# Kernel tuning notes

Hardware: AMD Instinct MI355X
Metric: run time of the kernel (lower is better)

The kernel has to match this reference:

```python
import jax, jax.numpy as jnp
import numpy as np

FP4_AMAX = 6.0
FP8_AMAX = 448.0
E2M1_LUT = jnp.array([0.0, 0.5, 1.0, 1.5, 2.0, 3.0, 4.0, 6.0], dtype=jnp.float32)
# (threshold, code) pairs; applied in order, alternating <= and < comparisons
THRESHOLDS = [(5.0, 6), (3.5, 5), (2.5, 4), (1.75, 3), (1.25, 2), (0.75, 1), (0.25, 0)]


def _fp4_code(a):
    # a: abs-values, float32. Round-to-e2m1 magnitude code per the torch threshold table.
    code = jnp.full(a.shape, 7, dtype=jnp.int32)
    for i, (m, c) in enumerate(THRESHOLDS):
        mask = (a <= m) if i % 2 == 0 else (a < m)
        code = jnp.where(mask, c, code)
    return code


def simulate_nvfp4_quantize(w):
    # w: (out, in), in % 16 == 0. Returns fake-quantized weight, same shape/dtype.
    out_f, in_f = w.shape
    wb = w.reshape(out_f, in_f // 16, 16).astype(jnp.float32)
    gs = (FP4_AMAX * FP8_AMAX) / jnp.max(jnp.abs(wb))          # global fp32 scale
    s_decb = jnp.max(jnp.abs(wb), axis=-1) / FP4_AMAX           # per-16-block decode scale
    xs = jnp.clip(s_decb * gs, -FP8_AMAX, FP8_AMAX).astype(jnp.float8_e4m3fn)  # fp8 block scales
    xs_f = xs.astype(jnp.float32)
    s_encb = gs / jnp.clip(xs_f, 1e-12, None)                   # encode scale per block
    x_scaled = wb * s_encb[..., None]
    sign = jnp.where(jnp.signbit(x_scaled), -1.0, 1.0)
    mag = E2M1_LUT[_fp4_code(jnp.abs(x_scaled))]
    wq = sign * mag * (xs_f / gs)[..., None]                    # dequantize
    return wq.reshape(out_f, in_f).astype(w.dtype)


def setup_inputs() -> dict:
    key = jax.random.key(0)
    k1, k2, k3 = jax.random.split(key, 3)
    B, S, IN, OUT = 4, 2048, 4096, 4096
    x = jax.random.normal(k1, (B, S, IN), dtype=jnp.float32)
    weight = jax.random.normal(k2, (OUT, IN), dtype=jnp.float32) * 0.02
    bias = jax.random.normal(k3, (OUT,), dtype=jnp.float32) * 0.01
    return {"x": x, "weight": weight, "bias": bias}


def reference(x, weight, bias):
    # STE quantization: forward uses fake-quant weight
    weight_q = simulate_nvfp4_quantize(weight)
    # F.linear: x @ W^T + b
    return jnp.einsum("bsi,oi->bso", x, weight_q) + bias
```

## Files before the change

### kernel.cpp

```cpp
#include <hip/hip_runtime.h>
#include <hip/hip_bf16.h>
#include <stdint.h>

typedef __bf16 bf16_t;
typedef __bf16 bf16x8 __attribute__((ext_vector_type(8)));
typedef float  f32x4  __attribute__((ext_vector_type(4)));

#define BM 256
#define BN 256
#define BK 64
#define NTHREADS 512

__global__ void k_absmax(const float* __restrict__ w, unsigned int* __restrict__ out_bits, int n4) {
    int i = blockIdx.x * blockDim.x + threadIdx.x;
    int stride = gridDim.x * blockDim.x;
    const float4* w4 = (const float4*)w;
    float m = 0.0f;
    for (; i < n4; i += stride) {
        float4 v = w4[i];
        m = fmaxf(m, fmaxf(fmaxf(fabsf(v.x), fabsf(v.y)), fmaxf(fabsf(v.z), fabsf(v.w))));
    }
    #pragma unroll
    for (int off = 32; off; off >>= 1)
        m = fmaxf(m, __shfl_xor(m, off));
    if ((threadIdx.x & 63) == 0)
        atomicMax(out_bits, __float_as_uint(m));
}

__device__ __forceinline__ float e4m3_rne(float v) {
    if (v < 0.015625f) {
        return rintf(v * 512.0f) * (1.0f / 512.0f);
    }
    unsigned int u = __float_as_uint(v);
    unsigned int keep = u >> 20;
    unsigned int r = u & 0xFFFFFu;
    if (r > 0x80000u || (r == 0x80000u && (keep & 1u))) keep++;
    return __uint_as_float(keep << 20);
}

__global__ void k_quantize(const float* __restrict__ w, bf16_t* __restrict__ wq,
                           const unsigned int* __restrict__ maxbits, int nblk) {
    int t = blockIdx.x * blockDim.x + threadIdx.x;
    if (t >= nblk) return;
    float gmax = __uint_as_float(*maxbits);
    float gs = 2688.0f / gmax;
    const float4* w4 = (const float4*)w + (size_t)t * 4;
    float4 v0 = w4[0], v1 = w4[1], v2 = w4[2], v3 = w4[3];
    float vv[16];
    vv[0]=v0.x; vv[1]=v0.y; vv[2]=v0.z; vv[3]=v0.w;
    vv[4]=v1.x; vv[5]=v1.y; vv[6]=v1.z; vv[7]=v1.w;
    vv[8]=v2.x; vv[9]=v2.y; vv[10]=v2.z; vv[11]=v2.w;
    vv[12]=v3.x; vv[13]=v3.y; vv[14]=v3.z; vv[15]=v3.w;
    float bmax = 0.0f;
    #pragma unroll
    for (int j = 0; j < 16; ++j) bmax = fmaxf(bmax, fabsf(vv[j]));
    float s_decb = bmax / 6.0f;
    float xs_in  = fminf(s_decb * gs, 448.0f);
    float xs_f   = e4m3_rne(xs_in);
    float s_encb = gs / fmaxf(xs_f, 1e-12f);
    float dscale = xs_f / gs;
    bf16x8 o0, o1;
    #pragma unroll
    for (int j = 0; j < 16; ++j) {
        float xsc = vv[j] * s_encb;
        float a = fabsf(xsc);
        float mag = (a <= 0.25f) ? 0.0f
                  : (a <  0.75f) ? 0.5f
                  : (a <= 1.25f) ? 1.0f
                  : (a <  1.75f) ? 1.5f
                  : (a <= 2.5f ) ? 2.0f
                  : (a <  3.5f ) ? 3.0f
                  : (a <= 5.0f ) ? 4.0f : 6.0f;
        float sgn = __builtin_copysignf(1.0f, xsc);
        float val = (sgn * mag) * dscale;
        if (j < 8) o0[j] = (bf16_t)val; else o1[j - 8] = (bf16_t)val;
    }
    *(bf16x8*)(wq + (size_t)t * 16)     = o0;
    *(bf16x8*)(wq + (size_t)t * 16 + 8) = o1;
}

__global__ void k_cvt_x(const float* __restrict__ x, bf16_t* __restrict__ xb, long n8) {
    long i = blockIdx.x * (long)blockDim.x + threadIdx.x;
    long stride = (long)gridDim.x * blockDim.x;
    const float4* x4 = (const float4*)x;
    for (; i < n8; i += stride) {
        float4 a = x4[2 * i], b = x4[2 * i + 1];
        bf16x8 o;
        o[0] = (bf16_t)a.x; o[1] = (bf16_t)a.y; o[2] = (bf16_t)a.z; o[3] = (bf16_t)a.w;
        o[4] = (bf16_t)b.x; o[5] = (bf16_t)b.y; o[6] = (bf16_t)b.z; o[7] = (bf16_t)b.w;
        *(bf16x8*)(xb + i * 8) = o;
    }
}

__device__ __forceinline__ void BARRIER() {
    asm volatile("" ::: "memory");
    __builtin_amdgcn_s_barrier();
    asm volatile("" ::: "memory");
}

__device__ __forceinline__ void gload16(const bf16_t* g, bf16_t* l) {
    __builtin_amdgcn_global_load_lds(
        (const __attribute__((address_space(1))) unsigned int*)g,
        (__attribute__((address_space(3))) unsigned int*)l,
        16, 0, 0);
}

__global__ __launch_bounds__(NTHREADS, 2) void k_gemm(
        const bf16_t* __restrict__ A,
        const bf16_t* __restrict__ Bt,
        const float*  __restrict__ bias,
        float* __restrict__ C, int M, int N, int K) {
    __shared__ __align__(16) bf16_t sA[2][BM * BK];
    __shared__ __align__(16) bf16_t sB[2][BN * BK];

    int bid = blockIdx.x;
    int cpx = gridDim.x >> 3;
    int swz = (bid & 7) * cpx + (bid >> 3);
    int nbn = N / BN;
    int m0 = (swz / nbn) * BM, n0 = (swz % nbn) * BN;

    int tid  = threadIdx.x;
    int lane = tid & 63;
    int w    = tid >> 6;
    int wr   = w >> 2, wc = w & 3;
    int fr15 = lane & 15;
    int kg   = lane >> 4;

    int rowin = tid >> 3;
    int pg    = tid & 7;
    int gsw   = pg ^ (rowin & 7);
    int gstg[2], lstg[2];
    #pragma unroll
    for (int l = 0; l < 2; ++l) {
        gstg[l] = (l * 128 + rowin) * K + gsw * 8;
        lstg[l] = (l * 128 + rowin) * 64 + pg * 8;
    }
    int tq0 = tid >> 8;
    int rB  = (tid >> 3) & 31;
    int gbstg[2], lbstg[2];
    #pragma unroll
    for (int l = 0; l < 2; ++l) {
        int q = l * 2 + tq0;
        gbstg[l] = (q * 64 + rB) * K + gsw * 8;
        lbstg[l] = (q * 64 + rB) * 64 + pg * 8;
    }
    const bf16_t* Ab = A  + (size_t)m0 * K;
    const bf16_t* Bb = Bt + (size_t)n0 * K;

#define STGA(BUF, H, KT) do {                                                      \
        gload16(Ab + (H) * 64 * K + gstg[0] + (KT), &sA[BUF][(H) * 4096 + lstg[0]]); \
        gload16(Ab + (H) * 64 * K + gstg[1] + (KT), &sA[BUF][(H) * 4096 + lstg[1]]); \
    } while (0)
#define STGB(BUF, H, KT) do {                                                      \
        gload16(Bb + (H) * 32 * K + gbstg[0] + (KT), &sB[BUF][(H) * 2048 + lbstg[0]]); \
        gload16(Bb + (H) * 32 * K + gbstg[1] + (KT), &sB[BUF][(H) * 2048 + lbstg[1]]); \
    } while (0)

    int f01 = fr15 & 3, f2 = (fr15 >> 2) & 1;
    int pgr0 = 4 * (0 ^ f2) + (kg ^ f01);
    int pgr1 = 4 * (1 ^ f2) + (kg ^ f01);
    int baseA0 = (wr * 128 + fr15) * 64 + pgr0 * 8;
    int baseA1 = (wr * 128 + fr15) * 64 + pgr1 * 8;
    int baseB0 = (wc * 64  + fr15) * 64 + pgr0 * 8;
    int baseB1 = (wc * 64  + fr15) * 64 + pgr1 * 8;

    f32x4 acc[8][4] = {};
    bf16x8 afr[4][2];
    bf16x8 bfr[4][2];

    const int NT = K / BK;
    const int ITERS = NT / 2;

    STGB(0, 0, 0);  STGB(0, 1, 0);
    STGA(0, 0, 0);  STGA(0, 1, 0);
    STGB(1, 0, BK); STGB(1, 1, BK);
    STGA(1, 0, BK);
    asm volatile("s_waitcnt vmcnt(6)" ::: "memory");
    BARRIER();

#define RDA4(PA, MH) do {                                                          \
        _Pragma("unroll")                                                          \
        for (int m = 0; m < 4; ++m)                                                \
            afr[m][0] = *(const bf16x8*)((PA) + baseA0 + ((MH) * 4 + m) * 1024);   \
        _Pragma("unroll")                                                          \
        for (int m = 0; m < 4; ++m)                                                \
            afr[m][1] = *(const bf16x8*)((PA) + baseA1 + ((MH) * 4 + m) * 1024);   \
    } while (0)

#define RDB2(PB, NH) do {                                                          \
        _Pragma("unroll")                                                          \
        for (int j = 0; j < 2; ++j)                                                \
            bfr[(NH)*2+j][0] = *(const bf16x8*)((PB) + baseB0 + ((NH)*2+j) * 1024);\
        _Pragma("unroll")                                                          \
        for (int j = 0; j < 2; ++j)                                                \
            bfr[(NH)*2+j][1] = *(const bf16x8*)((PB) + baseB1 + ((NH)*2+j) * 1024);\
    } while (0)

#define MFQ(MH, NH) do {                                                                            \
        __builtin_amdgcn_s_setprio(1);                                                              \
        _Pragma("unroll")                                                                           \
        for (int n = 0; n < 2; ++n)                                                                 \
            _Pragma("unroll")                                                                       \
            for (int m = 0; m < 4; ++m)                                                             \
                acc[(MH)*4+m][(NH)*2+n] = __builtin_amdgcn_mfma_f32_16x16x32_bf16(                  \
                    afr[m][0], bfr[(NH)*2+n][0], acc[(MH)*4+m][(NH)*2+n], 0, 0, 0);                 \
        _Pragma("unroll")                                                                           \
        for (int n = 0; n < 2; ++n)                                                                 \
            _Pragma("unroll")                                                                       \
            for (int m = 0; m < 4; ++m)                                                             \
                acc[(MH)*4+m][(NH)*2+n] = __builtin_amdgcn_mfma_f32_16x16x32_bf16(                  \
                    afr[m][1], bfr[(NH)*2+n][1], acc[(MH)*4+m][(NH)*2+n], 0, 0, 0);                 \
        __builtin_amdgcn_s_setprio(0);                                                              \
    } while (0)

    RDA4(sA[0], 0); RDB2(sB[0], 0);

    for (int it = 0; it < ITERS; ++it) {
        const bool nl = (it + 1 < ITERS);
        const int ktB1 = (2 * it + 1) * BK;
        const int kt2  = (2 * it + 2) * BK;
        const int kt3  = (2 * it + 3) * BK;

        MFQ(0, 0);
        RDB2(sB[0], 1);
        STGA(1, 1, ktB1);
        BARRIER();

        MFQ(0, 1);
        RDA4(sA[0], 1);
        if (nl) STGB(0, 0, kt2);
        BARRIER();

        MFQ(1, 0);
        if (nl) STGB(0, 1, kt2);
        if (nl) { asm volatile("s_waitcnt vmcnt(6)" ::: "memory"); }
        else    { asm volatile("s_waitcnt vmcnt(2)" ::: "memory"); }
        BARRIER();

        MFQ(1, 1);
        if (nl) STGA(0, 0, kt2);
        if (nl) { asm volatile("s_waitcnt vmcnt(6)" ::: "memory"); }
        else    { asm volatile("s_waitcnt vmcnt(0)" ::: "memory"); }
        RDA4(sA[1], 0); RDB2(sB[1], 0);
        BARRIER();

        MFQ(0, 0);
        RDB2(sB[1], 1);
        if (nl) STGA(0, 1, kt2);
        BARRIER();

        MFQ(0, 1);
        RDA4(sA[1], 1);
        if (nl) STGB(1, 0, kt3);
        BARRIER();

        MFQ(1, 0);
        if (nl) STGB(1, 1, kt3);
        asm volatile("s_waitcnt vmcnt(6)" ::: "memory");
        BARRIER();

        MFQ(1, 1);
        if (nl) {
            STGA(1, 0, kt3);
            asm volatile("s_waitcnt vmcnt(6)" ::: "memory");
            RDA4(sA[0], 0); RDB2(sB[0], 0);
        }
        BARRIER();
    }
    asm volatile("s_waitcnt vmcnt(0)" ::: "memory");

    int crow = (lane >> 4) * 4;
    int ccol = lane & 15;
    float bv[4];
    #pragma unroll
    for (int j = 0; j < 4; ++j) bv[j] = bias[n0 + wc * 64 + j * 16 + ccol];
    #pragma unroll
    for (int i = 0; i < 8; ++i) {
        size_t mrow = (size_t)(m0 + wr * 128 + i * 16 + crow);
        #pragma unroll
        for (int j = 0; j < 4; ++j) {
            float* cp = C + mrow * N + (n0 + wc * 64 + j * 16 + ccol);
            #pragma unroll
            for (int r = 0; r < 4; ++r)
                cp[(size_t)r * N] = acc[i][j][r] + bv[j];
        }
    }
#undef STGA
#undef STGB
#undef RDA4
#undef RDB2
#undef MFQ
}

extern "C" void kernel_launch(void* const* d_in, const int* in_sizes, int n_in,
                              void* d_out, int out_size, void* d_ws, size_t ws_size,
                              hipStream_t stream) {
    const float* x    = (const float*)d_in[0];
    const float* wgt  = (const float*)d_in[1];
    const float* bias = (const float*)d_in[2];
    float* out = (float*)d_out;

    const int N = in_sizes[2];
    const int K = in_sizes[1] / N;
    const int M = in_sizes[0] / K;

    unsigned int* maxbits = (unsigned int*)d_ws;
    bf16_t* wq = (bf16_t*)((char*)d_ws + 256);
    bf16_t* xb = (bf16_t*)((char*)d_ws + 256 + (size_t)N * K * sizeof(bf16_t));

    hipMemsetAsync(d_ws, 0, 256, stream);
    k_absmax<<<512, 256, 0, stream>>>(wgt, maxbits, N * K / 4);
    int nblk = N * K / 16;
    k_quantize<<<(nblk + 255) / 256, 256, 0, stream>>>(wgt, wq, maxbits, nblk);
    long n8 = (long)M * K / 8;
    k_cvt_x<<<2048, 256, 0, stream>>>(x, xb, n8);
    dim3 grid((M / BM) * (N / BN));
    k_gemm<<<grid, NTHREADS, 0, stream>>>(xb, wq, bias, out, M, N, K);
}
```

Before: 361.9 us.

## Double-buffer A fragments so LDS reads overlap MFMA in GEMM loop

Replaces the single A-fragment register set with two ping-pong sets (aX/aY). Each phase now issues the LDS reads for the next sub-tile and the global stage loads before its MFMA block instead of after it. The goal is to hide LDS read latency behind matrix-core work rather than stalling at each barrier. In exchange it uses roughly 32 more VGPRs per thread on top of the large accumulator array, which risks lower occupancy or register spills, and it reorders reads relative to the vmcnt waits.

```diff
diff --git a/kernel.cpp b/kernel.cpp
--- a/kernel.cpp
+++ b/kernel.cpp
@@ -165,7 +165,7 @@
     int baseB1 = (wc * 64  + fr15) * 64 + pgr1 * 8;
 
     f32x4 acc[8][4] = {};
-    bf16x8 afr[4][2];
+    bf16x8 aX[4][2], aY[4][2];
     bf16x8 bfr[4][2];
 
     const int NT = K / BK;
@@ -178,16 +178,16 @@
     asm volatile("s_waitcnt vmcnt(6)" ::: "memory");
     BARRIER();
 
-#define RDA4(PA, MH) do {                                                          \
+#define RDA(BK_, PA, MH) do {                                                      \
         _Pragma("unroll")                                                          \
         for (int m = 0; m < 4; ++m)                                                \
-            afr[m][0] = *(const bf16x8*)((PA) + baseA0 + ((MH) * 4 + m) * 1024);   \
+            BK_[m][0] = *(const bf16x8*)((PA) + baseA0 + ((MH) * 4 + m) * 1024);   \
         _Pragma("unroll")                                                          \
         for (int m = 0; m < 4; ++m)                                                \
-            afr[m][1] = *(const bf16x8*)((PA) + baseA1 + ((MH) * 4 + m) * 1024);   \
-    } while (0)
-
-#define RDB2(PB, NH) do {                                                          \
+            BK_[m][1] = *(const bf16x8*)((PA) + baseA1 + ((MH) * 4 + m) * 1024);   \
+    } while (0)
+
+#define RDB(PB, NH) do {                                                           \
         _Pragma("unroll")                                                          \
         for (int j = 0; j < 2; ++j)                                                \
             bfr[(NH)*2+j][0] = *(const bf16x8*)((PB) + baseB0 + ((NH)*2+j) * 1024);\
@@ -196,24 +196,25 @@
             bfr[(NH)*2+j][1] = *(const bf16x8*)((PB) + baseB1 + ((NH)*2+j) * 1024);\
     } while (0)
 
-#define MFQ(MH, NH) do {                                                                            \
+#define MFQ(BK_, MH, NH) do {                                                                       \
         __builtin_amdgcn_s_setprio(1);                                                              \
         _Pragma("unroll")                                                                           \
         for (int n = 0; n < 2; ++n)                                                                 \
             _Pragma("unroll")                                                                       \
             for (int m = 0; m < 4; ++m)                                                             \
                 acc[(MH)*4+m][(NH)*2+n] = __builtin_amdgcn_mfma_f32_16x16x32_bf16(                  \
-                    afr[m][0], bfr[(NH)*2+n][0], acc[(MH)*4+m][(NH)*2+n], 0, 0, 0);                 \
+                    BK_[m][0], bfr[(NH)*2+n][0], acc[(MH)*4+m][(NH)*2+n], 0, 0, 0);                 \
         _Pragma("unroll")                                                                           \
         for (int n = 0; n < 2; ++n)                                                                 \
             _Pragma("unroll")                                                                       \
             for (int m = 0; m < 4; ++m)                                                             \
                 acc[(MH)*4+m][(NH)*2+n] = __builtin_amdgcn_mfma_f32_16x16x32_bf16(                  \
-                    afr[m][1], bfr[(NH)*2+n][1], acc[(MH)*4+m][(NH)*2+n], 0, 0, 0);                 \
+                    BK_[m][1], bfr[(NH)*2+n][1], acc[(MH)*4+m][(NH)*2+n], 0, 0, 0);                 \
         __builtin_amdgcn_s_setprio(0);                                                              \
     } while (0)
 
-    RDA4(sA[0], 0); RDB2(sB[0], 0);
+    RDA(aX, sA[0], 0);
+    RDB(sB[0], 0);
 
     for (int it = 0; it < ITERS; ++it) {
         const bool nl = (it + 1 < ITERS);
@@ -221,49 +222,57 @@
         const int kt2  = (2 * it + 2) * BK;
         const int kt3  = (2 * it + 3) * BK;
 
-        MFQ(0, 0);
-        RDB2(sB[0], 1);
+        RDB(sB[0], 1);
         STGA(1, 1, ktB1);
-        BARRIER();
-
-        MFQ(0, 1);
-        RDA4(sA[0], 1);
+        MFQ(aX, 0, 0);
+        BARRIER();
+
+        RDA(aY, sA[0], 1);
         if (nl) STGB(0, 0, kt2);
-        BARRIER();
-
-        MFQ(1, 0);
+        MFQ(aX, 0, 1);
+        BARRIER();
+
         if (nl) STGB(0, 1, kt2);
+        MFQ(aY, 1, 0);
         if (nl) { asm volatile("s_waitcnt vmcnt(6)" ::: "memory"); }
         else    { asm volatile("s_waitcnt vmcnt(2)" ::: "memory"); }
         BARRIER();
 
-        MFQ(1, 1);
+        RDA(aX, sA[1], 0);
+        RDB(sB[1], 0);
         if (nl) STGA(0, 0, kt2);
+        MFQ(aY, 1, 1);
         if (nl) { asm volatile("s_waitcnt vmcnt(6)" ::: "memory"); }
         else    { asm volatile("s_waitcnt vmcnt(0)" ::: "memory"); }
-        RDA4(sA[1], 0); RDB2(sB[1], 0);
-        BARRIER();
-
-        MFQ(0, 0);
-        RDB2(sB[1], 1);
+        BARRIER();
+
+        RDB(sB[1], 1);
         if (nl) STGA(0, 1, kt2);
-        BARRIER();
-
-        MFQ(0, 1);
-        RDA4(sA[1], 1);
+        MFQ(aX, 0, 0);
+        BARRIER();
+
+        RDA(aY, sA[1], 1);
         if (nl) STGB(1, 0, kt3);
-        BARRIER();
-
-        MFQ(1, 0);
-        if (nl) STGB(1, 1, kt3);
-        asm volatile("s_waitcnt vmcnt(6)" ::: "memory");
-        BARRIER();
-
-        MFQ(1, 1);
+        MFQ(aX, 0, 1);
+        BARRIER();
+
         if (nl) {
+            STGB(1, 1, kt3);
+            MFQ(aY, 1, 0);
+            asm volatile("s_waitcnt vmcnt(6)" ::: "memory");
+        } else {
+            MFQ(aY, 1, 0);
+        }
+        BARRIER();
+
+        if (nl) {
+            RDA(aX, sA[0], 0);
+            RDB(sB[0], 0);
             STGA(1, 0, kt3);
+            MFQ(aY, 1, 1);
             asm volatile("s_waitcnt vmcnt(6)" ::: "memory");
-            RDA4(sA[0], 0); RDB2(sB[0], 0);
+        } else {
+            MFQ(aY, 1, 1);
         }
         BARRIER();
     }
@@ -287,8 +296,8 @@
     }
 #undef STGA
 #undef STGB
-#undef RDA4
-#undef RDB2
+#undef RDA
+#undef RDB
 #undef MFQ
 }
 
```

Result: slower. 1.182 ms (+226.7%).

## Merge weight absmax with x conversion and restructure GEMM LDS read schedule

Applied to the files above, without the earlier changes.

The weight absmax reduction and the fp32-to-bf16 conversion of x now share one launch, with blocks split by index, so the two memory-bound passes overlap and one launch goes away. The GEMM main loop is reordered so LDS fragment reads for each MFMA quarter are issued before it, with explicit lgkmcnt waits and extra barriers. This removes the prefetch of fragments during the previous quarter's MFMAs. It also doubles the barrier count, which can reduce overlap of LDS reads with matrix math.

```diff
diff --git a/kernel.cpp b/kernel.cpp
--- a/kernel.cpp
+++ b/kernel.cpp
@@ -11,20 +11,36 @@
 #define BK 64
 #define NTHREADS 512
 
-__global__ void k_absmax(const float* __restrict__ w, unsigned int* __restrict__ out_bits, int n4) {
-    int i = blockIdx.x * blockDim.x + threadIdx.x;
-    int stride = gridDim.x * blockDim.x;
-    const float4* w4 = (const float4*)w;
-    float m = 0.0f;
-    for (; i < n4; i += stride) {
-        float4 v = w4[i];
-        m = fmaxf(m, fmaxf(fmaxf(fabsf(v.x), fabsf(v.y)), fmaxf(fabsf(v.z), fabsf(v.w))));
-    }
-    #pragma unroll
-    for (int off = 32; off; off >>= 1)
-        m = fmaxf(m, __shfl_xor(m, off));
-    if ((threadIdx.x & 63) == 0)
-        atomicMax(out_bits, __float_as_uint(m));
+__global__ void k_absmax_cvt(const float* __restrict__ w, unsigned int* __restrict__ out_bits,
+                             int n4w, const float* __restrict__ x, bf16_t* __restrict__ xb,
+                             long n8x) {
+    int tid = threadIdx.x;
+    if (blockIdx.x < 512) {
+        int i = blockIdx.x * blockDim.x + tid;
+        int stride = 512 * blockDim.x;
+        const float4* w4 = (const float4*)w;
+        float m = 0.0f;
+        for (; i < n4w; i += stride) {
+            float4 v = w4[i];
+            m = fmaxf(m, fmaxf(fmaxf(fabsf(v.x), fabsf(v.y)), fmaxf(fabsf(v.z), fabsf(v.w))));
+        }
+        #pragma unroll
+        for (int off = 32; off; off >>= 1)
+            m = fmaxf(m, __shfl_xor(m, off));
+        if ((tid & 63) == 0)
+            atomicMax(out_bits, __float_as_uint(m));
+    } else {
+        long i = (long)(blockIdx.x - 512) * blockDim.x + tid;
+        long stride = 2048L * blockDim.x;
+        const float4* x4 = (const float4*)x;
+        for (; i < n8x; i += stride) {
+            float4 a = x4[2 * i], b = x4[2 * i + 1];
+            bf16x8 o;
+            o[0] = (bf16_t)a.x; o[1] = (bf16_t)a.y; o[2] = (bf16_t)a.z; o[3] = (bf16_t)a.w;
+            o[4] = (bf16_t)b.x; o[5] = (bf16_t)b.y; o[6] = (bf16_t)b.z; o[7] = (bf16_t)b.w;
+            *(bf16x8*)(xb + i * 8) = o;
+        }
+    }
 }
 
 __device__ __forceinline__ float e4m3_rne(float v) {
@@ -79,19 +95,6 @@
     *(bf16x8*)(wq + (size_t)t * 16 + 8) = o1;
 }
 
-__global__ void k_cvt_x(const float* __restrict__ x, bf16_t* __restrict__ xb, long n8) {
-    long i = blockIdx.x * (long)blockDim.x + threadIdx.x;
-    long stride = (long)gridDim.x * blockDim.x;
-    const float4* x4 = (const float4*)x;
-    for (; i < n8; i += stride) {
-        float4 a = x4[2 * i], b = x4[2 * i + 1];
-        bf16x8 o;
-        o[0] = (bf16_t)a.x; o[1] = (bf16_t)a.y; o[2] = (bf16_t)a.z; o[3] = (bf16_t)a.w;
-        o[4] = (bf16_t)b.x; o[5] = (bf16_t)b.y; o[6] = (bf16_t)b.z; o[7] = (bf16_t)b.w;
-        *(bf16x8*)(xb + i * 8) = o;
-    }
-}
-
 __device__ __forceinline__ void BARRIER() {
     asm volatile("" ::: "memory");
     __builtin_amdgcn_s_barrier();
@@ -178,7 +181,7 @@
     asm volatile("s_waitcnt vmcnt(6)" ::: "memory");
     BARRIER();
 
-#define RDA4(PA, MH) do {                                                          \
+#define RDA(PA, MH) do {                                                           \
         _Pragma("unroll")                                                          \
         for (int m = 0; m < 4; ++m)                                                \
             afr[m][0] = *(const bf16x8*)((PA) + baseA0 + ((MH) * 4 + m) * 1024);   \
@@ -187,7 +190,7 @@
             afr[m][1] = *(const bf16x8*)((PA) + baseA1 + ((MH) * 4 + m) * 1024);   \
     } while (0)
 
-#define RDB2(PB, NH) do {                                                          \
+#define RDB(PB, NH) do {                                                           \
         _Pragma("unroll")                                                          \
         for (int j = 0; j < 2; ++j)                                                \
             bfr[(NH)*2+j][0] = *(const bf16x8*)((PB) + baseB0 + ((NH)*2+j) * 1024);\
@@ -213,7 +216,8 @@
         __builtin_amdgcn_s_setprio(0);                                                              \
     } while (0)
 
-    RDA4(sA[0], 0); RDB2(sB[0], 0);
+#define LGKM0() asm volatile("s_waitcnt lgkmcnt(0)" ::: "memory")
+#define LGKM8() asm volatile("s_waitcnt lgkmcnt(8)" ::: "memory")
 
     for (int it = 0; it < ITERS; ++it) {
         const bool nl = (it + 1 < ITERS);
@@ -221,50 +225,55 @@
         const int kt2  = (2 * it + 2) * BK;
         const int kt3  = (2 * it + 3) * BK;
 
+        RDA(sA[0], 0); RDB(sB[0], 0);
+        STGA(1, 1, ktB1);
+        LGKM8();
+        BARRIER(); LGKM0();
         MFQ(0, 0);
-        RDB2(sB[0], 1);
-        STGA(1, 1, ktB1);
-        BARRIER();
-
+        BARRIER();
+
+        RDB(sB[0], 1);
+        if (nl) STGB(0, 0, kt2);
+        BARRIER(); LGKM0();
         MFQ(0, 1);
-        RDA4(sA[0], 1);
-        if (nl) STGB(0, 0, kt2);
-        BARRIER();
-
+        BARRIER();
+
+        RDA(sA[0], 1);
+        if (nl) STGB(0, 1, kt2);
+        BARRIER(); LGKM0();
         MFQ(1, 0);
-        if (nl) STGB(0, 1, kt2);
-        if (nl) { asm volatile("s_waitcnt vmcnt(6)" ::: "memory"); }
-        else    { asm volatile("s_waitcnt vmcnt(2)" ::: "memory"); }
-        BARRIER();
-
+        BARRIER();
+
+        if (nl) STGA(0, 0, kt2);
+        BARRIER();
         MFQ(1, 1);
-        if (nl) STGA(0, 0, kt2);
         if (nl) { asm volatile("s_waitcnt vmcnt(6)" ::: "memory"); }
         else    { asm volatile("s_waitcnt vmcnt(0)" ::: "memory"); }
-        RDA4(sA[1], 0); RDB2(sB[1], 0);
-        BARRIER();
-
+        BARRIER();
+
+        RDA(sA[1], 0); RDB(sB[1], 0);
+        if (nl) STGA(0, 1, kt2);
+        LGKM8();
+        BARRIER(); LGKM0();
         MFQ(0, 0);
-        RDB2(sB[1], 1);
-        if (nl) STGA(0, 1, kt2);
-        BARRIER();
-
+        BARRIER();
+
+        RDB(sB[1], 1);
+        if (nl) STGB(1, 0, kt3);
+        BARRIER(); LGKM0();
         MFQ(0, 1);
-        RDA4(sA[1], 1);
-        if (nl) STGB(1, 0, kt3);
-        BARRIER();
-
+        BARRIER();
+
+        RDA(sA[1], 1);
+        if (nl) STGB(1, 1, kt3);
+        BARRIER(); LGKM0();
         MFQ(1, 0);
-        if (nl) STGB(1, 1, kt3);
-        asm volatile("s_waitcnt vmcnt(6)" ::: "memory");
-        BARRIER();
-
+        BARRIER();
+
+        if (nl) STGA(1, 0, kt3);
+        BARRIER();
         MFQ(1, 1);
-        if (nl) {
-            STGA(1, 0, kt3);
-            asm volatile("s_waitcnt vmcnt(6)" ::: "memory");
-            RDA4(sA[0], 0); RDB2(sB[0], 0);
-        }
+        if (nl) { asm volatile("s_waitcnt vmcnt(6)" ::: "memory"); }
         BARRIER();
     }
     asm volatile("s_waitcnt vmcnt(0)" ::: "memory");
@@ -287,9 +296,11 @@
     }
 #undef STGA
 #undef STGB
-#undef RDA4
-#undef RDB2
+#undef RDA
+#undef RDB
 #undef MFQ
+#undef LGKM0
+#undef LGKM8
 }
 
 extern "C" void kernel_launch(void* const* d_in, const int* in_sizes, int n_in,
@@ -309,11 +320,10 @@
     bf16_t* xb = (bf16_t*)((char*)d_ws + 256 + (size_t)N * K * sizeof(bf16_t));
 
     hipMemsetAsync(d_ws, 0, 256, stream);
-    k_absmax<<<512, 256, 0, stream>>>(wgt, maxbits, N * K / 4);
+    long n8 = (long)M * K / 8;
+    k_absmax_cvt<<<2560, 256, 0, stream>>>(wgt, maxbits, N * K / 4, x, xb, n8);
     int nblk = N * K / 16;
     k_quantize<<<(nblk + 255) / 256, 256, 0, stream>>>(wgt, wq, maxbits, nblk);
-    long n8 = (long)M * K / 8;
-    k_cvt_x<<<2048, 256, 0, stream>>>(x, xb, n8);
     dim3 grid((M / BM) * (N / BN));
     k_gemm<<<grid, NTHREADS, 0, stream>>>(xb, wq, bias, out, M, N, K);
 }
```

Result: faster. 334.7 us (median of 2 runs) (-7.5%).
